# Kernel tuning notes

Measured on AMD Instinct MI355X. Metric: run time of the kernel, lower is better.

Reference implementation:

```python
import jax, jax.numpy as jnp
import numpy as np


def _grid_sample_bilinear(plane, xy):
    """torch grid_sample, mode=bilinear, padding_mode=zeros, align_corners=True.
    plane: (C, H, W); xy: (N, 2) with xy[:,0]->W axis, xy[:,1]->H axis, in [-1,1].
    Returns (N, C)."""
    C, H, W = plane.shape
    x = (xy[:, 0] + 1.0) * 0.5 * (W - 1)  # pixel coords, align_corners=True
    y = (xy[:, 1] + 1.0) * 0.5 * (H - 1)
    x0 = jnp.floor(x)
    y0 = jnp.floor(y)
    wx = x - x0
    wy = y - y0
    x0i = x0.astype(jnp.int32)
    y0i = y0.astype(jnp.int32)

    def gather(yi, xi):
        valid = ((yi >= 0) & (yi < H) & (xi >= 0) & (xi < W)).astype(plane.dtype)
        v = plane[:, jnp.clip(yi, 0, H - 1), jnp.clip(xi, 0, W - 1)]  # (C, N)
        return v * valid  # zeros padding

    out = (gather(y0i, x0i) * ((1 - wx) * (1 - wy))
           + gather(y0i, x0i + 1) * (wx * (1 - wy))
           + gather(y0i + 1, x0i) * ((1 - wx) * wy)
           + gather(y0i + 1, x0i + 1) * (wx * wy))  # (C, N)
    return out.T  # (N, C)


def _sample_plane_xtytxy(coords3d, plane_xtyt, plane_xy):
    # coords3d: (N, 3) = (x, y, t)
    xy = coords3d[:, 0:2]
    yt = coords3d[:, 1:3]
    xt = coords3d[:, jnp.array([0, 2])]
    f_xt = _grid_sample_bilinear(plane_xtyt[0], xt)
    f_yt = _grid_sample_bilinear(plane_xtyt[1], yt)
    f_xy = _grid_sample_bilinear(plane_xy[0], xy)
    return f_xt + f_yt + f_xy  # (N, feat_dim)  [sum over the 3 planes]


def setup_inputs() -> dict:
    key = jax.random.key(0)
    ks = jax.random.split(key, 10)
    N, FD = 2_000_000, 16
    x_res = [128, 256, 512]
    t_res = [16, 32, 64]
    inp = {
        "coords": jax.random.uniform(ks[0], (N, 3), jnp.float32, minval=-1.0, maxval=1.0),
    }
    for i, (rx, rt) in enumerate(zip(x_res, t_res)):
        inp[f"xtyt_{i}"] = jax.random.normal(ks[1 + 2 * i], (2, FD, rt, rx), jnp.float32) * 0.001
        inp[f"xy_{i}"] = jax.random.normal(ks[2 + 2 * i], (1, FD, rx, rx), jnp.float32) * 0.001
    width, out_dim = 32, 2
    inp["w1"] = jax.random.normal(ks[7], (FD * 3, width), jnp.float32) * (1.0 / np.sqrt(FD * 3))
    inp["b1"] = jnp.zeros((width,), jnp.float32)
    inp["w2"] = jax.random.normal(ks[8], (width, out_dim), jnp.float32) * (1.0 / np.sqrt(width))
    inp["b2"] = jnp.zeros((out_dim,), jnp.float32)
    return inp


def reference(coords, xtyt_0, xy_0, xtyt_1, xy_1, xtyt_2, xy_2, w1, b1, w2, b2):
    feats = jnp.concatenate([
        _sample_plane_xtytxy(coords, xtyt_0, xy_0),
        _sample_plane_xtytxy(coords, xtyt_1, xy_1),
        _sample_plane_xtytxy(coords, xtyt_2, xy_2),
    ], axis=-1)  # (N, 48)
    h = jax.nn.leaky_relu(feats @ w1 + b1, negative_slope=0.01)
    return jax.nn.sigmoid(h @ w2 + b2)  # (N, 2) in [0, 1]
```

## Files before the change

### kernel.cpp

```cpp
#include <hip/hip_runtime.h>
#include <hip/hip_bf16.h>

#define FD 16

typedef __attribute__((ext_vector_type(2))) float f32x2;
typedef __attribute__((ext_vector_type(4))) float f32x4;
typedef __attribute__((ext_vector_type(4))) unsigned int u32x4;

__device__ __forceinline__ unsigned char enc_e4m3(float v) {
  float sv = v * 32768.0f;
  unsigned int bits = __float_as_uint(sv);
  unsigned int s = (bits >> 24) & 0x80u;
  float a = fabsf(sv);
  if (a >= 448.0f) return (unsigned char)(s | 0x7Eu);
  unsigned int tb = __float_as_uint(a * 0x1p-120f);
  unsigned int lsb = (tb >> 20) & 1u;
  tb += 0x7FFFFu + lsb;
  unsigned int em = (tb >> 20) & 0x7Fu;
  if (em > 0x7Eu) em = 0x7Eu;
  return (unsigned char)(s | em);
}

__global__ __launch_bounds__(256) void pack_kernel(
    const float* __restrict__ in, unsigned char* __restrict__ out,
    int P, int H, int W)
{
  int idx = blockIdx.x * blockDim.x + threadIdx.x;
  int total = P * H * W;
  if (idx >= total) return;
  int w  = idx % W;
  int ph = idx / W;
  int h  = ph % H;
  int p  = ph / H;
  int hw = H * W;
  const float* src = in + ((size_t)(p * FD) * H + h) * (size_t)W + w;
  unsigned int words[4];
#pragma unroll
  for (int g = 0; g < 4; ++g) {
    unsigned int acc = 0;
#pragma unroll
    for (int c = 0; c < 4; ++c) {
      unsigned int b = enc_e4m3(src[(size_t)(4 * g + c) * hw]);
      acc |= b << (8 * c);
    }
    words[g] = acc;
  }
  u32x4 v; v.x = words[0]; v.y = words[1]; v.z = words[2]; v.w = words[3];
  *(u32x4*)(out + (size_t)idx * FD) = v;
}

template<int H, int W>
__device__ __forceinline__ void sample_add(
    const unsigned char* __restrict__ base, float u, float v, f32x2* __restrict__ f)
{
  float gx = ((u + 1.0f) * 0.5f) * (float)(W - 1);
  float gy = ((v + 1.0f) * 0.5f) * (float)(H - 1);
  float fx0 = floorf(gx), fy0 = floorf(gy);
  float wx = gx - fx0, wy = gy - fy0;
  int x0 = (int)fx0, y0 = (int)fy0;
  int x0c = min(max(x0, 0), W - 1);
  int x1c = min(max(x0 + 1, 0), W - 1);
  int y0c = min(max(y0, 0), H - 1);
  int y1c = min(max(y0 + 1, 0), H - 1);
  float w00 = (1.0f - wx) * (1.0f - wy);
  float w01 = wx * (1.0f - wy);
  float w10 = (1.0f - wx) * wy;
  float w11 = wx * wy;
  u32x4 A = *(const u32x4*)(base + ((y0c * W + x0c) << 4));
  u32x4 B = *(const u32x4*)(base + ((y0c * W + x1c) << 4));
  u32x4 C = *(const u32x4*)(base + ((y1c * W + x0c) << 4));
  u32x4 D = *(const u32x4*)(base + ((y1c * W + x1c) << 4));
  f32x2 vw00 = {w00, w00}, vw01 = {w01, w01}, vw10 = {w10, w10}, vw11 = {w11, w11};
#pragma unroll
  for (int g = 0; g < 4; ++g) {
    f32x2 acc0 = f[2 * g + 0];
    f32x2 acc1 = f[2 * g + 1];
    acc0 = __builtin_elementwise_fma(vw00, __builtin_amdgcn_cvt_pk_f32_fp8(A[g], false), acc0);
    acc1 = __builtin_elementwise_fma(vw00, __builtin_amdgcn_cvt_pk_f32_fp8(A[g], true ), acc1);
    acc0 = __builtin_elementwise_fma(vw01, __builtin_amdgcn_cvt_pk_f32_fp8(B[g], false), acc0);
    acc1 = __builtin_elementwise_fma(vw01, __builtin_amdgcn_cvt_pk_f32_fp8(B[g], true ), acc1);
    acc0 = __builtin_elementwise_fma(vw10, __builtin_amdgcn_cvt_pk_f32_fp8(C[g], false), acc0);
    acc1 = __builtin_elementwise_fma(vw10, __builtin_amdgcn_cvt_pk_f32_fp8(C[g], true ), acc1);
    acc0 = __builtin_elementwise_fma(vw11, __builtin_amdgcn_cvt_pk_f32_fp8(D[g], false), acc0);
    acc1 = __builtin_elementwise_fma(vw11, __builtin_amdgcn_cvt_pk_f32_fp8(D[g], true ), acc1);
    f[2 * g + 0] = acc0;
    f[2 * g + 1] = acc1;
  }
}

__device__ __forceinline__ void mlp_chunk(
    const f32x2* __restrict__ fr, const float* __restrict__ s_w1, int row0,
    f32x2* __restrict__ h2)
{
#pragma unroll
  for (int k = 0; k < 16; ++k) {
    float fk = fr[k >> 1][k & 1];
    f32x2 fk2 = {fk, fk};
    const f32x4* wrow = (const f32x4*)(s_w1 + (row0 + k) * 32);
#pragma unroll
    for (int q = 0; q < 8; ++q) {
      f32x4 w4 = wrow[q];
      f32x2 wlo = {w4.x, w4.y};
      f32x2 whi = {w4.z, w4.w};
      h2[2 * q + 0] = __builtin_elementwise_fma(fk2, wlo, h2[2 * q + 0]);
      h2[2 * q + 1] = __builtin_elementwise_fma(fk2, whi, h2[2 * q + 1]);
    }
  }
}

constexpr int SZ0_XT = 2 * 16 * 128 * FD;
constexpr int SZ0_XY = 128 * 128 * FD;
constexpr int SZ1_XT = 2 * 32 * 256 * FD;
constexpr int SZ1_XY = 256 * 256 * FD;
constexpr int SZ2_XT = 2 * 64 * 512 * FD;
constexpr int SZ2_XY = 512 * 512 * FD;
constexpr int OFF0_XT = 0;
constexpr int OFF0_XY = OFF0_XT + SZ0_XT;
constexpr int OFF1_XT = OFF0_XY + SZ0_XY;
constexpr int OFF1_XY = OFF1_XT + SZ1_XT;
constexpr int OFF2_XT = OFF1_XY + SZ1_XY;
constexpr int OFF2_XY = OFF2_XT + SZ2_XT;

__global__ __launch_bounds__(256) void triplane_kernel(
    const float* __restrict__ coords,
    const unsigned char* __restrict__ planes,
    const float* __restrict__ w1, const float* __restrict__ b1,
    const float* __restrict__ w2, const float* __restrict__ b2,
    float* __restrict__ out, int N)
{
  __shared__ __align__(16) float s_w1[48 * 32];
  __shared__ float s_b1[32];
  __shared__ float s_w2t[2 * 32];
  __shared__ float s_b2[2];
  for (int i = threadIdx.x; i < 48 * 32; i += 256) s_w1[i] = w1[i] * 0x1p-15f;
  if (threadIdx.x < 32) s_b1[threadIdx.x] = b1[threadIdx.x];
  if (threadIdx.x < 64) {
    int j = threadIdx.x >> 1, c = threadIdx.x & 1;
    s_w2t[c * 32 + j] = w2[j * 2 + c];
  }
  if (threadIdx.x < 2)  s_b2[threadIdx.x] = b2[threadIdx.x];
  __syncthreads();

  int n = blockIdx.x * blockDim.x + threadIdx.x;
  if (n >= N) return;

  float x = coords[3 * (size_t)n + 0];
  float y = coords[3 * (size_t)n + 1];
  float t = coords[3 * (size_t)n + 2];

  f32x2 h2[16];
#pragma unroll
  for (int j = 0; j < 16; ++j) { h2[j][0] = s_b1[2 * j]; h2[j][1] = s_b1[2 * j + 1]; }

  {
    f32x2 fr[8];
#pragma unroll
    for (int i = 0; i < 8; ++i) { fr[i][0] = 0.0f; fr[i][1] = 0.0f; }
    sample_add<16, 128>(planes + OFF0_XT,                 x, t, fr);
    sample_add<16, 128>(planes + OFF0_XT + 16 * 128 * FD, y, t, fr);
    sample_add<128, 128>(planes + OFF0_XY,                x, y, fr);
    mlp_chunk(fr, s_w1, 0, h2);
  }
  {
    f32x2 fr[8];
#pragma unroll
    for (int i = 0; i < 8; ++i) { fr[i][0] = 0.0f; fr[i][1] = 0.0f; }
    sample_add<32, 256>(planes + OFF1_XT,                 x, t, fr);
    sample_add<32, 256>(planes + OFF1_XT + 32 * 256 * FD, y, t, fr);
    sample_add<256, 256>(planes + OFF1_XY,                x, y, fr);
    mlp_chunk(fr, s_w1, 16, h2);
  }
  {
    f32x2 fr[8];
#pragma unroll
    for (int i = 0; i < 8; ++i) { fr[i][0] = 0.0f; fr[i][1] = 0.0f; }
    sample_add<64, 512>(planes + OFF2_XT,                 x, t, fr);
    sample_add<64, 512>(planes + OFF2_XT + 64 * 512 * FD, y, t, fr);
    sample_add<512, 512>(planes + OFF2_XY,                x, y, fr);
    mlp_chunk(fr, s_w1, 32, h2);
  }

  f32x2 zero = {0.0f, 0.0f};
  f32x2 c01 = {0.01f, 0.01f};
#pragma unroll
  for (int j = 0; j < 16; ++j) {
    f32x2 hp = __builtin_elementwise_max(h2[j], zero);
    f32x2 hn = __builtin_elementwise_min(h2[j], zero);
    h2[j] = __builtin_elementwise_fma(c01, hn, hp);
  }

  f32x2 oa = zero, ob = zero;
#pragma unroll
  for (int j = 0; j < 16; ++j) {
    f32x2 w2a = *(const f32x2*)(s_w2t + 2 * j);
    f32x2 w2b = *(const f32x2*)(s_w2t + 32 + 2 * j);
    oa = __builtin_elementwise_fma(h2[j], w2a, oa);
    ob = __builtin_elementwise_fma(h2[j], w2b, ob);
  }
  float o0 = s_b2[0] + oa[0] + oa[1];
  float o1 = s_b2[1] + ob[0] + ob[1];

  f32x2 r;
  r[0] = 1.0f / (1.0f + __expf(-o0));
  r[1] = 1.0f / (1.0f + __expf(-o1));
  *(f32x2*)(out + 2 * (size_t)n) = r;
}

extern "C" void kernel_launch(void* const* d_in, const int* in_sizes, int n_in,
                              void* d_out, int out_size, void* d_ws, size_t ws_size,
                              hipStream_t stream) {
  const float* coords = (const float*)d_in[0];
  const float* xtyt0  = (const float*)d_in[1];
  const float* xy0    = (const float*)d_in[2];
  const float* xtyt1  = (const float*)d_in[3];
  const float* xy1    = (const float*)d_in[4];
  const float* xtyt2  = (const float*)d_in[5];
  const float* xy2    = (const float*)d_in[6];
  const float* w1     = (const float*)d_in[7];
  const float* b1     = (const float*)d_in[8];
  const float* w2     = (const float*)d_in[9];
  const float* b2     = (const float*)d_in[10];

  unsigned char* planes = (unsigned char*)d_ws;
  const int N = in_sizes[0] / 3;

  auto launch_pk = [&](const float* src, int off, int P, int H, int W) {
    int total = P * H * W;
    int blocks = (total + 255) / 256;
    hipLaunchKernelGGL(pack_kernel, dim3(blocks), dim3(256), 0, stream,
                       src, planes + off, P, H, W);
  };
  launch_pk(xtyt0, OFF0_XT, 2, 16, 128);
  launch_pk(xy0,   OFF0_XY, 1, 128, 128);
  launch_pk(xtyt1, OFF1_XT, 2, 32, 256);
  launch_pk(xy1,   OFF1_XY, 1, 256, 256);
  launch_pk(xtyt2, OFF2_XT, 2, 64, 512);
  launch_pk(xy2,   OFF2_XY, 1, 512, 512);

  int blocks = (N + 255) / 256;
  hipLaunchKernelGGL(triplane_kernel, dim3(blocks), dim3(256), 0, stream,
                     coords, planes, w1, b1, w2, b2, (float*)d_out, N);
}
```

Baseline: 353.4 us.

## Bucket-sort points spatially before sampling and merge plane pack launches

Adds a counting sort of the query points into 32K spatial buckets (histogram, single-block scan, atomic scatter), so that the sampling kernel processes spatially nearby points together and gets better cache locality on the plane gathers. Output is scattered back to each point's original index. The six pack launches are also merged into one kernel. The cost is four extra passes over the coordinates plus atomics and a serial scan. The sorted path is used only when the workspace is large enough; otherwise it falls back to direct processing.

```diff
diff --git a/kernel.cpp b/kernel.cpp
--- a/kernel.cpp
+++ b/kernel.cpp
@@ -21,32 +21,124 @@
   return (unsigned char)(s | em);
 }
 
-__global__ __launch_bounds__(256) void pack_kernel(
-    const float* __restrict__ in, unsigned char* __restrict__ out,
-    int P, int H, int W)
-{
-  int idx = blockIdx.x * blockDim.x + threadIdx.x;
-  int total = P * H * W;
-  if (idx >= total) return;
-  int w  = idx % W;
-  int ph = idx / W;
-  int h  = ph % H;
-  int p  = ph / H;
-  int hw = H * W;
-  const float* src = in + ((size_t)(p * FD) * H + h) * (size_t)W + w;
+constexpr int SZ0_XT = 2 * 16 * 128 * FD;
+constexpr int SZ0_XY = 128 * 128 * FD;
+constexpr int SZ1_XT = 2 * 32 * 256 * FD;
+constexpr int SZ1_XY = 256 * 256 * FD;
+constexpr int SZ2_XT = 2 * 64 * 512 * FD;
+constexpr int SZ2_XY = 512 * 512 * FD;
+constexpr int OFF0_XT = 0;
+constexpr int OFF0_XY = OFF0_XT + SZ0_XT;
+constexpr int OFF1_XT = OFF0_XY + SZ0_XY;
+constexpr int OFF1_XY = OFF1_XT + SZ1_XT;
+constexpr int OFF2_XT = OFF1_XY + SZ1_XY;
+constexpr int OFF2_XY = OFF2_XT + SZ2_XT;
+constexpr size_t PLANES_BYTES = (size_t)OFF2_XY + SZ2_XY;
+
+constexpr int NBUCKETS = 1 << 15;
+constexpr size_t HIST_OFF = PLANES_BYTES;
+constexpr size_t SORT_OFF = HIST_OFF + (size_t)NBUCKETS * 4;
+
+constexpr int NB0_XT = (2 * 16 * 128) / 256;
+constexpr int NB0_XY = (128 * 128) / 256;
+constexpr int NB1_XT = (2 * 32 * 256) / 256;
+constexpr int NB1_XY = (256 * 256) / 256;
+constexpr int NB2_XT = (2 * 64 * 512) / 256;
+constexpr int NB2_XY = (512 * 512) / 256;
+constexpr int B0 = 0;
+constexpr int B1 = B0 + NB0_XT;
+constexpr int B2 = B1 + NB0_XY;
+constexpr int B3 = B2 + NB1_XT;
+constexpr int B4 = B3 + NB1_XY;
+constexpr int B5 = B4 + NB2_XT;
+constexpr int B6 = B5 + NB2_XY;
+
+__global__ __launch_bounds__(256) void pack_all_kernel(
+    const float* __restrict__ s0, const float* __restrict__ s1,
+    const float* __restrict__ s2, const float* __restrict__ s3,
+    const float* __restrict__ s4, const float* __restrict__ s5,
+    unsigned char* __restrict__ planes)
+{
+  int bid = blockIdx.x;
+  const float* src; int off, H, W, base;
+  if      (bid < B1) { src = s0; off = OFF0_XT; H = 16;  W = 128; base = B0; }
+  else if (bid < B2) { src = s1; off = OFF0_XY; H = 128; W = 128; base = B1; }
+  else if (bid < B3) { src = s2; off = OFF1_XT; H = 32;  W = 256; base = B2; }
+  else if (bid < B4) { src = s3; off = OFF1_XY; H = 256; W = 256; base = B3; }
+  else if (bid < B5) { src = s4; off = OFF2_XT; H = 64;  W = 512; base = B4; }
+  else               { src = s5; off = OFF2_XY; H = 512; W = 512; base = B5; }
+  int idx = (bid - base) * 256 + threadIdx.x;
+  int hw  = H * W;
+  int w   = idx % W;
+  int ph  = idx / W;
+  int h   = ph % H;
+  int p   = ph / H;
+  const float* sp = src + ((size_t)(p * FD) * H + h) * (size_t)W + w;
   unsigned int words[4];
 #pragma unroll
   for (int g = 0; g < 4; ++g) {
     unsigned int acc = 0;
 #pragma unroll
     for (int c = 0; c < 4; ++c) {
-      unsigned int b = enc_e4m3(src[(size_t)(4 * g + c) * hw]);
+      unsigned int b = enc_e4m3(sp[(size_t)(4 * g + c) * hw]);
       acc |= b << (8 * c);
     }
     words[g] = acc;
   }
   u32x4 v; v.x = words[0]; v.y = words[1]; v.z = words[2]; v.w = words[3];
-  *(u32x4*)(out + (size_t)idx * FD) = v;
+  *(u32x4*)(planes + off + (size_t)idx * FD) = v;
+}
+
+__device__ __forceinline__ int bucket_key(float x, float y, float t) {
+  int qx = min(63, max(0, (int)((x + 1.0f) * 32.0f)));
+  int qy = min(63, max(0, (int)((y + 1.0f) * 32.0f)));
+  int qt = min(7,  max(0, (int)((t + 1.0f) * 4.0f)));
+  return (qt << 12) | (qy << 6) | qx;
+}
+
+__global__ __launch_bounds__(256) void hist_kernel(
+    const float* __restrict__ coords, unsigned int* __restrict__ hist, int N)
+{
+  int n = blockIdx.x * blockDim.x + threadIdx.x;
+  if (n >= N) return;
+  const float* c = coords + 3 * (size_t)n;
+  atomicAdd(&hist[bucket_key(c[0], c[1], c[2])], 1u);
+}
+
+__global__ __launch_bounds__(1024) void scan_kernel(unsigned int* __restrict__ hist)
+{
+  __shared__ unsigned int s[1024];
+  int tid = threadIdx.x;
+  int base = tid * 32;
+  unsigned int loc[32];
+  unsigned int sum = 0;
+#pragma unroll
+  for (int i = 0; i < 32; ++i) { loc[i] = hist[base + i]; sum += loc[i]; }
+  s[tid] = sum;
+  __syncthreads();
+  for (int off = 1; off < 1024; off <<= 1) {
+    unsigned int v = 0;
+    if (tid >= off) v = s[tid - off];
+    __syncthreads();
+    s[tid] += v;
+    __syncthreads();
+  }
+  unsigned int run = (tid > 0) ? s[tid - 1] : 0u;
+#pragma unroll
+  for (int i = 0; i < 32; ++i) { unsigned int c = loc[i]; hist[base + i] = run; run += c; }
+}
+
+__global__ __launch_bounds__(256) void scatter_kernel(
+    const float* __restrict__ coords, unsigned int* __restrict__ hist,
+    float* __restrict__ sorted, int N)
+{
+  int n = blockIdx.x * blockDim.x + threadIdx.x;
+  if (n >= N) return;
+  const float* c = coords + 3 * (size_t)n;
+  float x = c[0], y = c[1], t = c[2];
+  unsigned int pos = atomicAdd(&hist[bucket_key(x, y, t)], 1u);
+  f32x4 v; v.x = x; v.y = y; v.z = t; v.w = __uint_as_float((unsigned int)n);
+  *(f32x4*)(sorted + 4 * (size_t)pos) = v;
 }
 
 template<int H, int W>
@@ -108,102 +200,107 @@
   }
 }
 
-constexpr int SZ0_XT = 2 * 16 * 128 * FD;
-constexpr int SZ0_XY = 128 * 128 * FD;
-constexpr int SZ1_XT = 2 * 32 * 256 * FD;
-constexpr int SZ1_XY = 256 * 256 * FD;
-constexpr int SZ2_XT = 2 * 64 * 512 * FD;
-constexpr int SZ2_XY = 512 * 512 * FD;
-constexpr int OFF0_XT = 0;
-constexpr int OFF0_XY = OFF0_XT + SZ0_XT;
-constexpr int OFF1_XT = OFF0_XY + SZ0_XY;
-constexpr int OFF1_XY = OFF1_XT + SZ1_XT;
-constexpr int OFF2_XT = OFF1_XY + SZ1_XY;
-constexpr int OFF2_XY = OFF2_XT + SZ2_XT;
-
-__global__ __launch_bounds__(256) void triplane_kernel(
+__device__ __forceinline__ void triplane_point(
+    float x, float y, float t,
+    const unsigned char* __restrict__ planes,
+    const float* __restrict__ s_w1, const float* __restrict__ s_b1,
+    const float* __restrict__ s_w2t, const float* __restrict__ s_b2,
+    float* __restrict__ out, size_t outIdx)
+{
+  f32x2 h2[16];
+#pragma unroll
+  for (int j = 0; j < 16; ++j) { h2[j][0] = s_b1[2 * j]; h2[j][1] = s_b1[2 * j + 1]; }
+
+  {
+    f32x2 fr[8];
+#pragma unroll
+    for (int i = 0; i < 8; ++i) fr[i] = (f32x2){0.f, 0.f};
+    sample_add<16, 128>(planes + OFF0_XT,                 x, t, fr);
+    sample_add<16, 128>(planes + OFF0_XT + 16 * 128 * FD, y, t, fr);
+    sample_add<128, 128>(planes + OFF0_XY,                x, y, fr);
+    mlp_chunk(fr, s_w1, 0, h2);
+  }
+  {
+    f32x2 fr[8];
+#pragma unroll
+    for (int i = 0; i < 8; ++i) fr[i] = (f32x2){0.f, 0.f};
+    sample_add<32, 256>(planes + OFF1_XT,                 x, t, fr);
+    sample_add<32, 256>(planes + OFF1_XT + 32 * 256 * FD, y, t, fr);
+    sample_add<256, 256>(planes + OFF1_XY,                x, y, fr);
+    mlp_chunk(fr, s_w1, 16, h2);
+  }
+  {
+    f32x2 fr[8];
+#pragma unroll
+    for (int i = 0; i < 8; ++i) fr[i] = (f32x2){0.f, 0.f};
+    sample_add<64, 512>(planes + OFF2_XT,                 x, t, fr);
+    sample_add<64, 512>(planes + OFF2_XT + 64 * 512 * FD, y, t, fr);
+    sample_add<512, 512>(planes + OFF2_XY,                x, y, fr);
+    mlp_chunk(fr, s_w1, 32, h2);
+  }
+
+  f32x2 zero = {0.0f, 0.0f};
+  f32x2 c01 = {0.01f, 0.01f};
+  f32x2 oa = zero, ob = zero;
+#pragma unroll
+  for (int j = 0; j < 16; ++j) {
+    f32x2 hp = __builtin_elementwise_max(h2[j], zero);
+    f32x2 hn = __builtin_elementwise_min(h2[j], zero);
+    f32x2 hj = __builtin_elementwise_fma(c01, hn, hp);
+    f32x2 w2a = *(const f32x2*)(s_w2t + 2 * j);
+    f32x2 w2b = *(const f32x2*)(s_w2t + 32 + 2 * j);
+    oa = __builtin_elementwise_fma(hj, w2a, oa);
+    ob = __builtin_elementwise_fma(hj, w2b, ob);
+  }
+  float o0 = s_b2[0] + oa[0] + oa[1];
+  float o1 = s_b2[1] + ob[0] + ob[1];
+  f32x2 r;
+  r[0] = 1.0f / (1.0f + __expf(-o0));
+  r[1] = 1.0f / (1.0f + __expf(-o1));
+  *(f32x2*)(out + 2 * outIdx) = r;
+}
+
+#define LOAD_WEIGHTS                                                          \
+  __shared__ __align__(16) float s_w1[48 * 32];                               \
+  __shared__ float s_b1[32];                                                  \
+  __shared__ float s_w2t[2 * 32];                                             \
+  __shared__ float s_b2[2];                                                   \
+  for (int i = threadIdx.x; i < 48 * 32; i += 256) s_w1[i] = w1[i] * 0x1p-15f;\
+  if (threadIdx.x < 32) s_b1[threadIdx.x] = b1[threadIdx.x];                  \
+  if (threadIdx.x < 64) {                                                     \
+    int j = threadIdx.x >> 1, c = threadIdx.x & 1;                            \
+    s_w2t[c * 32 + j] = w2[j * 2 + c];                                        \
+  }                                                                           \
+  if (threadIdx.x < 2) s_b2[threadIdx.x] = b2[threadIdx.x];                   \
+  __syncthreads();
+
+__global__ __launch_bounds__(256) void triplane_sorted_kernel(
+    const float* __restrict__ sorted,
+    const unsigned char* __restrict__ planes,
+    const float* __restrict__ w1, const float* __restrict__ b1,
+    const float* __restrict__ w2, const float* __restrict__ b2,
+    float* __restrict__ out, int N)
+{
+  LOAD_WEIGHTS
+  int n = blockIdx.x * blockDim.x + threadIdx.x;
+  if (n >= N) return;
+  f32x4 c = *(const f32x4*)(sorted + 4 * (size_t)n);
+  unsigned int orig = __float_as_uint(c.w);
+  triplane_point(c.x, c.y, c.z, planes, s_w1, s_b1, s_w2t, s_b2, out, (size_t)orig);
+}
+
+__global__ __launch_bounds__(256) void triplane_direct_kernel(
     const float* __restrict__ coords,
     const unsigned char* __restrict__ planes,
     const float* __restrict__ w1, const float* __restrict__ b1,
     const float* __restrict__ w2, const float* __restrict__ b2,
     float* __restrict__ out, int N)
 {
-  __shared__ __align__(16) float s_w1[48 * 32];
-  __shared__ float s_b1[32];
-  __shared__ float s_w2t[2 * 32];
-  __shared__ float s_b2[2];
-  for (int i = threadIdx.x; i < 48 * 32; i += 256) s_w1[i] = w1[i] * 0x1p-15f;
-  if (threadIdx.x < 32) s_b1[threadIdx.x] = b1[threadIdx.x];
-  if (threadIdx.x < 64) {
-    int j = threadIdx.x >> 1, c = threadIdx.x & 1;
-    s_w2t[c * 32 + j] = w2[j * 2 + c];
-  }
-  if (threadIdx.x < 2)  s_b2[threadIdx.x] = b2[threadIdx.x];
-  __syncthreads();
-
+  LOAD_WEIGHTS
   int n = blockIdx.x * blockDim.x + threadIdx.x;
   if (n >= N) return;
-
-  float x = coords[3 * (size_t)n + 0];
-  float y = coords[3 * (size_t)n + 1];
-  float t = coords[3 * (size_t)n + 2];
-
-  f32x2 h2[16];
-#pragma unroll
-  for (int j = 0; j < 16; ++j) { h2[j][0] = s_b1[2 * j]; h2[j][1] = s_b1[2 * j + 1]; }
-
-  {
-    f32x2 fr[8];
-#pragma unroll
-    for (int i = 0; i < 8; ++i) { fr[i][0] = 0.0f; fr[i][1] = 0.0f; }
-    sample_add<16, 128>(planes + OFF0_XT,                 x, t, fr);
-    sample_add<16, 128>(planes + OFF0_XT + 16 * 128 * FD, y, t, fr);
-    sample_add<128, 128>(planes + OFF0_XY,                x, y, fr);
-    mlp_chunk(fr, s_w1, 0, h2);
-  }
-  {
-    f32x2 fr[8];
-#pragma unroll
-    for (int i = 0; i < 8; ++i) { fr[i][0] = 0.0f; fr[i][1] = 0.0f; }
-    sample_add<32, 256>(planes + OFF1_XT,                 x, t, fr);
-    sample_add<32, 256>(planes + OFF1_XT + 32 * 256 * FD, y, t, fr);
-    sample_add<256, 256>(planes + OFF1_XY,                x, y, fr);
-    mlp_chunk(fr, s_w1, 16, h2);
-  }
-  {
-    f32x2 fr[8];
-#pragma unroll
-    for (int i = 0; i < 8; ++i) { fr[i][0] = 0.0f; fr[i][1] = 0.0f; }
-    sample_add<64, 512>(planes + OFF2_XT,                 x, t, fr);
-    sample_add<64, 512>(planes + OFF2_XT + 64 * 512 * FD, y, t, fr);
-    sample_add<512, 512>(planes + OFF2_XY,                x, y, fr);
-    mlp_chunk(fr, s_w1, 32, h2);
-  }
-
-  f32x2 zero = {0.0f, 0.0f};
-  f32x2 c01 = {0.01f, 0.01f};
-#pragma unroll
-  for (int j = 0; j < 16; ++j) {
-    f32x2 hp = __builtin_elementwise_max(h2[j], zero);
-    f32x2 hn = __builtin_elementwise_min(h2[j], zero);
-    h2[j] = __builtin_elementwise_fma(c01, hn, hp);
-  }
-
-  f32x2 oa = zero, ob = zero;
-#pragma unroll
-  for (int j = 0; j < 16; ++j) {
-    f32x2 w2a = *(const f32x2*)(s_w2t + 2 * j);
-    f32x2 w2b = *(const f32x2*)(s_w2t + 32 + 2 * j);
-    oa = __builtin_elementwise_fma(h2[j], w2a, oa);
-    ob = __builtin_elementwise_fma(h2[j], w2b, ob);
-  }
-  float o0 = s_b2[0] + oa[0] + oa[1];
-  float o1 = s_b2[1] + ob[0] + ob[1];
-
-  f32x2 r;
-  r[0] = 1.0f / (1.0f + __expf(-o0));
-  r[1] = 1.0f / (1.0f + __expf(-o1));
-  *(f32x2*)(out + 2 * (size_t)n) = r;
+  const float* cp = coords + 3 * (size_t)n;
+  triplane_point(cp[0], cp[1], cp[2], planes, s_w1, s_b1, s_w2t, s_b2, out, (size_t)n);
 }
 
 extern "C" void kernel_launch(void* const* d_in, const int* in_sizes, int n_in,
@@ -221,23 +318,29 @@
   const float* w2     = (const float*)d_in[9];
   const float* b2     = (const float*)d_in[10];
 
-  unsigned char* planes = (unsigned char*)d_ws;
+  unsigned char* ws = (unsigned char*)d_ws;
+  unsigned char* planes = ws;
   const int N = in_sizes[0] / 3;
 
-  auto launch_pk = [&](const float* src, int off, int P, int H, int W) {
-    int total = P * H * W;
-    int blocks = (total + 255) / 256;
-    hipLaunchKernelGGL(pack_kernel, dim3(blocks), dim3(256), 0, stream,
-                       src, planes + off, P, H, W);
-  };
-  launch_pk(xtyt0, OFF0_XT, 2, 16, 128);
-  launch_pk(xy0,   OFF0_XY, 1, 128, 128);
-  launch_pk(xtyt1, OFF1_XT, 2, 32, 256);
-  launch_pk(xy1,   OFF1_XY, 1, 256, 256);
-  launch_pk(xtyt2, OFF2_XT, 2, 64, 512);
-  launch_pk(xy2,   OFF2_XY, 1, 512, 512);
-
-  int blocks = (N + 255) / 256;
-  hipLaunchKernelGGL(triplane_kernel, dim3(blocks), dim3(256), 0, stream,
-                     coords, planes, w1, b1, w2, b2, (float*)d_out, N);
-}
+  hipLaunchKernelGGL(pack_all_kernel, dim3(B6), dim3(256), 0, stream,
+                     xtyt0, xy0, xtyt1, xy1, xtyt2, xy2, planes);
+
+  const size_t needed = SORT_OFF + (size_t)N * 16;
+  const int pblocks = (N + 255) / 256;
+
+  if (ws_size >= needed) {
+    unsigned int* hist = (unsigned int*)(ws + HIST_OFF);
+    float* sorted = (float*)(ws + SORT_OFF);
+    hipMemsetAsync(hist, 0, (size_t)NBUCKETS * 4, stream);
+    hipLaunchKernelGGL(hist_kernel, dim3(pblocks), dim3(256), 0, stream,
+                       coords, hist, N);
+    hipLaunchKernelGGL(scan_kernel, dim3(1), dim3(1024), 0, stream, hist);
+    hipLaunchKernelGGL(scatter_kernel, dim3(pblocks), dim3(256), 0, stream,
+                       coords, hist, sorted, N);
+    hipLaunchKernelGGL(triplane_sorted_kernel, dim3(pblocks), dim3(256), 0, stream,
+                       sorted, planes, w1, b1, w2, b2, (float*)d_out, N);
+  } else {
+    hipLaunchKernelGGL(triplane_direct_kernel, dim3(pblocks), dim3(256), 0, stream,
+                       coords, planes, w1, b1, w2, b2, (float*)d_out, N);
+  }
+}
```

Result: slower. 477.0 us (+35.0%).
